# Kernel tuning notes

Measured on AMD Instinct MI355X. Metric: run time of the kernel, lower is better.

## Reference

```python
import jax, jax.numpy as jnp
import numpy as np

B, L, HIDDEN = 64, 200, 256
HEADS = 8
MAX_WIDTH = 5
EPS = 1e-5  # F.layer_norm default eps


def _ln(x):
    # F.layer_norm with no learned affine
    m = jnp.mean(x, axis=-1, keepdims=True)
    v = jnp.mean((x - m) ** 2, axis=-1, keepdims=True)
    return (x - m) * jax.lax.rsqrt(v + EPS)


def _area_pool(x, max_width, mode):
    # x: [B, H, L, D] -> pooled spans of widths 1..max_width (valid windows),
    # concatenated along the memory axis: M = sum_w (L - w + 1)
    Lx = x.shape[2]
    outs = []
    for w in range(1, max_width + 1):
        # [w, B, H, L-w+1, D] stack of shifted slices (w <= 5, tiny loop)
        win = jnp.stack([x[:, :, i:Lx - w + 1 + i, :] for i in range(w)], axis=0)
        if mode == 'max':
            outs.append(win.max(axis=0))
        elif mode == 'mean':
            outs.append(win.mean(axis=0))
        else:  # 'sum'
            outs.append(win.sum(axis=0))
    return jnp.concatenate(outs, axis=2)


def _mha_area(q_in, k_in, v_in, Wq, bq, Wk, bk, Wv, bv, Wo, bo):
    # per-head size equals hidden_size (key_query_size_hidden = hidden_size)
    Bq, Lq, _ = q_in.shape
    Dh = Wq.shape[1] // HEADS

    def split(x):
        return x.reshape(x.shape[0], x.shape[1], HEADS, Dh).transpose(0, 2, 1, 3)

    q = split(q_in @ Wq + bq)  # [B, H, Lq, Dh]
    k = split(k_in @ Wk + bk)
    v = split(v_in @ Wv + bv)
    k_area = _area_pool(k, MAX_WIDTH, 'max')   # aggr='max' key pooling
    v_area = _area_pool(v, MAX_WIDTH, 'sum')   # values pooled by sum (t2t default)
    scale = jnp.asarray(1.0 / np.sqrt(Dh), q.dtype)
    logits = jnp.einsum('bhqd,bhmd->bhqm', q, k_area) * scale
    attn = jax.nn.softmax(logits, axis=-1)  # dropout inactive at eval
    out = jnp.einsum('bhqm,bhmd->bhqd', attn, v_area)
    out = out.transpose(0, 2, 1, 3).reshape(Bq, Lq, HEADS * Dh)
    return out @ Wo + bo


def setup_inputs() -> dict:
    key = jax.random.key(0)
    ks = jax.random.split(key, 16)
    stdv = 1.0 / np.sqrt(HIDDEN)
    u = lambda k, shp: jax.random.uniform(k, shp, jnp.float32, -stdv, stdv)
    HD = HEADS * HIDDEN  # 2048
    return {
        'A': jax.random.normal(ks[0], (B, L, L), jnp.float32),
        'hidden': jax.random.normal(ks[1], (B, L, HIDDEN), jnp.float32),
        'Wq': u(ks[2], (HIDDEN, HD)), 'bq': u(ks[3], (HD,)),
        'Wk': u(ks[4], (HIDDEN, HD)), 'bk': u(ks[5], (HD,)),
        'Wv': u(ks[6], (HIDDEN, HD)), 'bv': u(ks[7], (HD,)),
        'Wo': u(ks[8], (HD, HIDDEN)), 'bo': u(ks[9], (HIDDEN,)),
        'W1': u(ks[10], (HIDDEN, 4 * HIDDEN)), 'b1': u(ks[11], (4 * HIDDEN,)),
        'W2': u(ks[12], (4 * HIDDEN, HIDDEN)), 'b2': u(ks[13], (HIDDEN,)),
    }


def reference(A, hidden, Wq, bq, Wk, bk, Wv, bv, Wo, bo, W1, b1, W2, b2):
    # step = 1 -> single ATTNCell; A is unused by ATTNCell (matches source)
    attn1 = _mha_area(hidden, hidden, hidden, Wq, bq, Wk, bk, Wv, bv, Wo, bo)
    attn1 = _ln(attn1 + hidden)
    attn2 = _mha_area(attn1, hidden, hidden, Wq, bq, Wk, bk, Wv, bv, Wo, bo)
    attn2 = _ln(attn1 + attn2)  # F.dropout inactive (eval)
    x = jax.nn.relu(attn2 @ W1 + b1) @ W2 + b2
    return _ln(attn2 + x)
```

## Files before the change

### kernel.cpp

```cpp
#include <hip/hip_runtime.h>
#include <hip/hip_bf16.h>
#include <cstdint>
#include <cstddef>

#define BATCH 64
#define LSEQ 200
#define HID 256
#define NH 8
#define DH 256
#define HD (NH*DH)
#define MROWS (BATCH*LSEQ)
#define EPS 1e-5f
#define CSCALE 0.09014195f

typedef unsigned short ushort_t;
typedef __attribute__((ext_vector_type(8))) short bf16x8;
typedef __attribute__((ext_vector_type(8))) unsigned short u16x8;
typedef __attribute__((ext_vector_type(4))) float f32x4;

__device__ __forceinline__ float b2f(ushort_t u) {
    union { unsigned int i; float f; } c; c.i = ((unsigned int)u) << 16; return c.f;
}
__device__ __forceinline__ ushort_t f2b(float f) {
    __hip_bfloat16 h = __float2bfloat16(f);
    union { __hip_bfloat16 h; ushort_t u; } c; c.h = h; return c.u;
}
__device__ __forceinline__ float to_f32(float x) { return x; }
__device__ __forceinline__ float to_f32(ushort_t x) { return b2f(x); }
__device__ __forceinline__ void store_val(float* p, float v) { *p = v; }
__device__ __forceinline__ void store_val(ushort_t* p, float v) { *p = f2b(v); }

__device__ __forceinline__ u16x8 bmax8(u16x8 a, u16x8 b) {
    union U { u16x8 v; __hip_bfloat162 h[4]; };
    U ua, ub, r; ua.v = a; ub.v = b;
    #pragma unroll
    for (int i = 0; i < 4; ++i) r.h[i] = __hmax2(ua.h[i], ub.h[i]);
    return r.v;
}

__device__ __forceinline__ void gll16(const void* g, void* l) {
    __builtin_amdgcn_global_load_lds(
        (const __attribute__((address_space(1))) unsigned int*)g,
        (__attribute__((address_space(3))) unsigned int*)l, 16, 0, 0);
}

template<bool RELU, bool SCALEC>
__global__ __launch_bounds__(256) void gemm_bt(
    const ushort_t* __restrict__ A, const ushort_t* __restrict__ Bt,
    const float* __restrict__ bias, ushort_t* __restrict__ C,
    int M, int N, int K)
{
    __shared__ ushort_t As[128 * 64];
    __shared__ ushort_t Bs[128 * 64];
    const int t = threadIdx.x;
    const int m0 = blockIdx.y * 128, n0 = blockIdx.x * 128;
    const int wave = t >> 6, lane = t & 63;
    const int l15 = lane & 15, lq = lane >> 4;
    const int wr = wave >> 1, wc = wave & 1;

    f32x4 acc[4][4];
    #pragma unroll
    for (int i = 0; i < 4; ++i)
        #pragma unroll
        for (int j = 0; j < 4; ++j) acc[i][j] = (f32x4){0.f, 0.f, 0.f, 0.f};

    for (int k0 = 0; k0 < K; k0 += 64) {
        __syncthreads();
        #pragma unroll
        for (int i = 0; i < 4; ++i) {
            int li = i * 256 + t;
            int ml = li >> 3, cp = li & 7;
            int cg = cp ^ (ml & 7);
            gll16(A + (size_t)(m0 + ml) * K + k0 + cg * 8, &As[li * 8]);
        }
        #pragma unroll
        for (int i = 0; i < 4; ++i) {
            int li = i * 256 + t;
            int nl = li >> 3, cp = li & 7;
            int cg = cp ^ (nl & 7);
            gll16(Bt + (size_t)(n0 + nl) * K + k0 + cg * 8, &Bs[li * 8]);
        }
        __syncthreads();
        #pragma unroll
        for (int ks = 0; ks < 2; ++ks) {
            bf16x8 af[4], bfr[4];
            #pragma unroll
            for (int i = 0; i < 4; ++i) {
                int r = wr * 64 + i * 16 + l15;
                int pc = (ks * 4 + lq) ^ (r & 7);
                af[i] = *(const bf16x8*)&As[r * 64 + pc * 8];
            }
            #pragma unroll
            for (int j = 0; j < 4; ++j) {
                int r = wc * 64 + j * 16 + l15;
                int pc = (ks * 4 + lq) ^ (r & 7);
                bfr[j] = *(const bf16x8*)&Bs[r * 64 + pc * 8];
            }
            #pragma unroll
            for (int i = 0; i < 4; ++i)
                #pragma unroll
                for (int j = 0; j < 4; ++j)
                    acc[i][j] = __builtin_amdgcn_mfma_f32_16x16x32_bf16(af[i], bfr[j], acc[i][j], 0, 0, 0);
        }
    }
    #pragma unroll
    for (int i = 0; i < 4; ++i) {
        #pragma unroll
        for (int e = 0; e < 4; ++e) {
            int m = m0 + wr * 64 + i * 16 + 4 * lq + e;
            #pragma unroll
            for (int j = 0; j < 4; ++j) {
                int n = n0 + wc * 64 + j * 16 + l15;
                float v = acc[i][j][e] + bias[n];
                if (RELU) v = fmaxf(v, 0.f);
                if (SCALEC) v *= CSCALE;
                C[(size_t)m * N + n] = f2b(v);
            }
        }
    }
}

__global__ __launch_bounds__(256) void gemm_qkv(
    const ushort_t* __restrict__ A, const ushort_t* __restrict__ Bt,
    const float* __restrict__ bq, const float* __restrict__ bk,
    const float* __restrict__ bv,
    ushort_t* __restrict__ Cq, ushort_t* __restrict__ Ck, ushort_t* __restrict__ Cv)
{
    constexpr int K = HID;
    __shared__ ushort_t As[128 * 64];
    __shared__ ushort_t Bs[128 * 64];
    const int t = threadIdx.x;
    const int m0 = blockIdx.y * 128, n0 = blockIdx.x * 128;
    const int wave = t >> 6, lane = t & 63;
    const int l15 = lane & 15, lq = lane >> 4;
    const int wr = wave >> 1, wc = wave & 1;

    f32x4 acc[4][4];
    #pragma unroll
    for (int i = 0; i < 4; ++i)
        #pragma unroll
        for (int j = 0; j < 4; ++j) acc[i][j] = (f32x4){0.f, 0.f, 0.f, 0.f};

    for (int k0 = 0; k0 < K; k0 += 64) {
        __syncthreads();
        #pragma unroll
        for (int i = 0; i < 4; ++i) {
            int li = i * 256 + t;
            int ml = li >> 3, cp = li & 7;
            int cg = cp ^ (ml & 7);
            gll16(A + (size_t)(m0 + ml) * K + k0 + cg * 8, &As[li * 8]);
        }
        #pragma unroll
        for (int i = 0; i < 4; ++i) {
            int li = i * 256 + t;
            int nl = li >> 3, cp = li & 7;
            int cg = cp ^ (nl & 7);
            gll16(Bt + (size_t)(n0 + nl) * K + k0 + cg * 8, &Bs[li * 8]);
        }
        __syncthreads();
        #pragma unroll
        for (int ks = 0; ks < 2; ++ks) {
            bf16x8 af[4], bfr[4];
            #pragma unroll
            for (int i = 0; i < 4; ++i) {
                int r = wr * 64 + i * 16 + l15;
                int pc = (ks * 4 + lq) ^ (r & 7);
                af[i] = *(const bf16x8*)&As[r * 64 + pc * 8];
            }
            #pragma unroll
            for (int j = 0; j < 4; ++j) {
                int r = wc * 64 + j * 16 + l15;
                int pc = (ks * 4 + lq) ^ (r & 7);
                bfr[j] = *(const bf16x8*)&Bs[r * 64 + pc * 8];
            }
            #pragma unroll
            for (int i = 0; i < 4; ++i)
                #pragma unroll
                for (int j = 0; j < 4; ++j)
                    acc[i][j] = __builtin_amdgcn_mfma_f32_16x16x32_bf16(af[i], bfr[j], acc[i][j], 0, 0, 0);
        }
    }

    const int seg = n0 >> 11;
    const int nb = n0 & 2047;
    if (seg == 2) {
        #pragma unroll
        for (int i = 0; i < 4; ++i) {
            int mbase = m0 + wr * 64 + i * 16 + 4 * lq;
            int bb = (int)(((unsigned)mbase * 5243u) >> 20);
            int ll = mbase - bb * 200;
            #pragma unroll
            for (int j = 0; j < 4; ++j) {
                int nn = nb + wc * 64 + j * 16 + l15;
                float bsv = bv[nn];
                ushort4 o4;
                o4.x = f2b(acc[i][j][0] + bsv); o4.y = f2b(acc[i][j][1] + bsv);
                o4.z = f2b(acc[i][j][2] + bsv); o4.w = f2b(acc[i][j][3] + bsv);
                size_t addr = ((size_t)(bb * NH + (nn >> 8)) * 256 + (nn & 255)) * LSEQ + ll;
                *(ushort4*)&Cv[addr] = o4;
            }
        }
    } else if (seg == 1) {
        #pragma unroll
        for (int i = 0; i < 4; ++i) {
            #pragma unroll
            for (int e = 0; e < 4; ++e) {
                int m = m0 + wr * 64 + i * 16 + 4 * lq + e;
                int bb = (int)(((unsigned)m * 5243u) >> 20);
                int ll = m - bb * 200;
                #pragma unroll
                for (int j = 0; j < 4; ++j) {
                    int nn = nb + wc * 64 + j * 16 + l15;
                    float v = acc[i][j][e] + bk[nn];
                    size_t addr = ((((size_t)(bb * NH + (nn >> 8))) * LSEQ + ll) << 8) + (nn & 255);
                    Ck[addr] = f2b(v);
                }
            }
        }
    } else {
        #pragma unroll
        for (int i = 0; i < 4; ++i) {
            #pragma unroll
            for (int e = 0; e < 4; ++e) {
                int m = m0 + wr * 64 + i * 16 + 4 * lq + e;
                #pragma unroll
                for (int j = 0; j < 4; ++j) {
                    int nn = nb + wc * 64 + j * 16 + l15;
                    float v = (acc[i][j][e] + bq[nn]) * CSCALE;
                    Cq[(size_t)m * HD + nn] = f2b(v);
                }
            }
        }
    }
}

__global__ __launch_bounds__(256) void gemm_bt64(
    const ushort_t* __restrict__ A, const ushort_t* __restrict__ Bt,
    const float* __restrict__ bias, ushort_t* __restrict__ C,
    int M, int N, int K)
{
    __shared__ ushort_t As[64 * 64];
    __shared__ ushort_t Bs[128 * 64];
    const int t = threadIdx.x;
    const int m0 = blockIdx.y * 64, n0 = blockIdx.x * 128;
    const int wave = t >> 6, lane = t & 63;
    const int l15 = lane & 15, lq = lane >> 4;
    const int wr = wave >> 1, wc = wave & 1;

    f32x4 acc[2][4];
    #pragma unroll
    for (int i = 0; i < 2; ++i)
        #pragma unroll
        for (int j = 0; j < 4; ++j) acc[i][j] = (f32x4){0.f, 0.f, 0.f, 0.f};

    for (int k0 = 0; k0 < K; k0 += 64) {
        __syncthreads();
        #pragma unroll
        for (int i = 0; i < 2; ++i) {
            int li = i * 256 + t;
            int ml = li >> 3, cp = li & 7;
            int cg = cp ^ (ml & 7);
            gll16(A + (size_t)(m0 + ml) * K + k0 + cg * 8, &As[li * 8]);
        }
        #pragma unroll
        for (int i = 0; i < 4; ++i) {
            int li = i * 256 + t;
            int nl = li >> 3, cp = li & 7;
            int cg = cp ^ (nl & 7);
            gll16(Bt + (size_t)(n0 + nl) * K + k0 + cg * 8, &Bs[li * 8]);
        }
        __syncthreads();
        #pragma unroll
        for (int ks = 0; ks < 2; ++ks) {
            bf16x8 af[2], bfr[4];
            #pragma unroll
            for (int i = 0; i < 2; ++i) {
                int r = wr * 32 + i * 16 + l15;
                int pc = (ks * 4 + lq) ^ (r & 7);
                af[i] = *(const bf16x8*)&As[r * 64 + pc * 8];
            }
            #pragma unroll
            for (int j = 0; j < 4; ++j) {
                int r = wc * 64 + j * 16 + l15;
                int pc = (ks * 4 + lq) ^ (r & 7);
                bfr[j] = *(const bf16x8*)&Bs[r * 64 + pc * 8];
            }
            #pragma unroll
            for (int i = 0; i < 2; ++i)
                #pragma unroll
                for (int j = 0; j < 4; ++j)
                    acc[i][j] = __builtin_amdgcn_mfma_f32_16x16x32_bf16(af[i], bfr[j], acc[i][j], 0, 0, 0);
        }
    }
    #pragma unroll
    for (int i = 0; i < 2; ++i) {
        #pragma unroll
        for (int e = 0; e < 4; ++e) {
            int m = m0 + wr * 32 + i * 16 + 4 * lq + e;
            #pragma unroll
            for (int j = 0; j < 4; ++j) {
                int n = n0 + wc * 64 + j * 16 + l15;
                C[(size_t)m * N + n] = f2b(acc[i][j][e] + bias[n]);
            }
        }
    }
}

__global__ __launch_bounds__(512, 2) void attn_mfma21(
    const ushort_t* __restrict__ Q, const ushort_t* __restrict__ Khm,
    const ushort_t* __restrict__ Vt, ushort_t* __restrict__ O)
{
    const int id = blockIdx.x;
    const int xcd = id & 7, slot_ = id >> 3;
    const int qt = slot_ & 1;
    const int bh = ((slot_ >> 1) << 3) + xcd;
    const int b = bh >> 3, h = bh & 7;
    const int q0 = qt * 128;
    const int t = threadIdx.x;
    const int wave = t >> 6, lane = t & 63;
    const int l15 = lane & 15, lq = lane >> 4;

    __shared__ ushort_t Ks[64 * 256];
    __shared__ ushort_t Vs[256 * 64];

    const ushort_t* kbh = Khm + (size_t)bh * LSEQ * DH;
    const ushort_t* vtb = Vt + (size_t)bh * DH * LSEQ;
    const ushort_t* qbh = Q + ((size_t)b * LSEQ) * HD + h * DH;
    const int qrow = q0 + wave * 16 + l15;

    bf16x8 qf[8];
    if (qrow < LSEQ) {
        const ushort_t* qp = qbh + (size_t)qrow * HD + 8 * lq;
        #pragma unroll
        for (int g = 0; g < 8; ++g) qf[g] = *(const bf16x8*)(qp + 32 * g);
    } else {
        bf16x8 zf = {0,0,0,0,0,0,0,0};
        #pragma unroll
        for (int g = 0; g < 8; ++g) qf[g] = zf;
    }

    f32x4 oacc[16];
    #pragma unroll
    for (int i = 0; i < 16; ++i) oacc[i] = (f32x4){0.f, 0.f, 0.f, 0.f};
    float l4[4];
    #pragma unroll
    for (int e = 0; e < 4; ++e) l4[e] = 0.f;
    float carry[4];
    #pragma unroll
    for (int e = 0; e < 4; ++e) carry[e] = 0.f;
    float Pagg[4][4];

    const int dc = t & 31, mb = t >> 5;
    const int vd = t >> 1, vh = t & 1;
    const int srow = ((mb >> 2) << 4) + (mb & 3);

    auto kOff = [&](int k4) {
        int m = mb + 16 * k4;
        return m * 256 + ((dc ^ (m & 15)) * 8);
    };
    auto storeVchunk = [&](int kc, u16x8 val) {
        *(u16x8*)&Vs[vd * 64 + ((kc ^ (vd & 7)) * 8)] = val;
    };

    auto qk = [&](f32x4* sacc) {
        __builtin_amdgcn_s_setprio(1);
        #pragma unroll
        for (int ms = 0; ms < 4; ++ms) {
            f32x4 s = (f32x4){0.f, 0.f, 0.f, 0.f};
            const int row = ms * 16 + l15;
            #pragma unroll
            for (int g = 0; g < 8; ++g) {
                const int phys = (lq + 4 * g) ^ l15;
                s = __builtin_amdgcn_mfma_f32_16x16x32_bf16(
                        *(const bf16x8*)&Ks[row * 256 + phys * 8], qf[g], s, 0, 0, 0);
            }
            sacc[ms] = s;
        }
        __builtin_amdgcn_s_setprio(0);
    };

    auto smClass = [&](const f32x4* sacc, int cls) {
        float Pc[4][4];
        #pragma unroll
        for (int ms = 0; ms < 4; ++ms)
            #pragma unroll
            for (int e = 0; e < 4; ++e) {
                float pe = __builtin_exp2f(sacc[ms][e]);
                l4[e] += pe;
                Pc[ms][e] = pe;
                Pagg[ms][e] += pe;
            }
        if (cls >= 1) {
            float T[4][4];
            #pragma unroll
            for (int ms = 0; ms < 4; ++ms)
                #pragma unroll
                for (int e = 0; e < 4; ++e) T[ms][e] = Pc[ms][e];
            #pragma unroll
            for (int u = 1; u <= 4; ++u) {
                if (u <= cls) {
                    float up = __shfl(T[3][3], (lane - 16) & 63);
                    #pragma unroll
                    for (int ms = 3; ms >= 0; --ms) {
                        float nv = (ms > 0) ? T[ms - 1][3] : ((lq > 0) ? up : 0.f);
                        T[ms][3] = T[ms][2]; T[ms][2] = T[ms][1]; T[ms][1] = T[ms][0];
                        T[ms][0] = nv;
                    }
                    #pragma unroll
                    for (int ms = 0; ms < 4; ++ms)
                        #pragma unroll
                        for (int e = 0; e < 4; ++e) Pagg[ms][e] += T[ms][e];
                }
            }
        }
        #pragma unroll
        for (int i = 0; i < 4; ++i)
            #pragma unroll
            for (int e = 0; e < 4; ++e)
                if (cls >= 4 + i - e) carry[i] += Pc[3][e];
    };

    auto pv32 = [&](const float P[4][4]) {
        unsigned int w[8];
        #pragma unroll
        for (int ms = 0; ms < 4; ++ms) {
            asm("v_cvt_pk_bf16_f32 %0, %1, %2" : "=v"(w[2*ms])   : "v"(P[ms][0]), "v"(P[ms][1]));
            asm("v_cvt_pk_bf16_f32 %0, %1, %2" : "=v"(w[2*ms+1]) : "v"(P[ms][2]), "v"(P[ms][3]));
        }
        union FR { unsigned int u[4]; bf16x8 v; };
        FR f0, f1;
        f0.u[0] = w[0]; f0.u[1] = w[1]; f0.u[2] = w[2]; f0.u[3] = w[3];
        f1.u[0] = w[4]; f1.u[1] = w[5]; f1.u[2] = w[6]; f1.u[3] = w[7];
        const bf16x8 pf0 = f0.v, pf1 = f1.v;
        __builtin_amdgcn_s_setprio(1);
        #pragma unroll
        for (int dt = 0; dt < 16; ++dt) {
            const int d = dt * 16 + l15;
            const int p0 = lq ^ (d & 7);
            const int p1 = (lq + 4) ^ (d & 7);
            oacc[dt] = __builtin_amdgcn_mfma_f32_16x16x32_bf16(
                           pf0, *(const bf16x8*)&Vs[d * 64 + p0 * 8], oacc[dt], 0, 0, 0);
            oacc[dt] = __builtin_amdgcn_mfma_f32_16x16x32_bf16(
                           pf1, *(const bf16x8*)&Vs[d * 64 + p1 * 8], oacc[dt], 0, 0, 0);
        }
        __builtin_amdgcn_s_setprio(0);
    };

    for (int ti = 0; ti < 3; ++ti) {
        const int st0 = ti * 64;
        {
            float pin0 = __shfl(carry[0], (lane + 48) & 63);
            float pin1 = __shfl(carry[1], (lane + 48) & 63);
            float pin2 = __shfl(carry[2], (lane + 48) & 63);
            float pin3 = __shfl(carry[3], (lane + 48) & 63);
            #pragma unroll
            for (int ms = 0; ms < 4; ++ms)
                #pragma unroll
                for (int e = 0; e < 4; ++e) Pagg[ms][e] = 0.f;
            if (lq == 0) {
                Pagg[0][0] = pin0; Pagg[0][1] = pin1; Pagg[0][2] = pin2; Pagg[0][3] = pin3;
            }
            #pragma unroll
            for (int e = 0; e < 4; ++e) carry[e] = 0.f;
        }
        #pragma unroll
        for (int cls = 0; cls < 5; ++cls) {
            u16x8 kf[4];
            #pragma unroll
            for (int k4 = 0; k4 < 4; ++k4)
                kf[k4] = *(const u16x8*)(kbh + (size_t)(st0 + srow + 4 * k4 + cls) * DH + dc * 8);
            u16x8 vc[4];
            if (cls == 0) {
                const ushort_t* vrow = vtb + (size_t)vd * LSEQ + st0 + vh * 32;
                #pragma unroll
                for (int c2 = 0; c2 < 4; ++c2) vc[c2] = *(const u16x8*)(vrow + c2 * 8);
            }
            __syncthreads();

            #pragma unroll
            for (int k4 = 0; k4 < 4; ++k4) {
                ushort_t* kp = &Ks[kOff(k4)];
                *(u16x8*)kp = (cls == 0) ? kf[k4] : bmax8(*(const u16x8*)kp, kf[k4]);
            }
            if (cls == 0) {
                #pragma unroll
                for (int cl = 0; cl < 4; ++cl) {
                    const int cg = vh * 4 + cl;
                    storeVchunk((cg & 1) * 4 + (cg >> 1), vc[cl]);
                }
            }
            __syncthreads();

            f32x4 sacc[4];
            qk(sacc);
            smClass(sacc, cls);
            if (cls == 4) pv32(Pagg);
        }
    }

    {
        __syncthreads();
        if (mb < 8) {
            u16x8 krun = *(const u16x8*)(kbh + (size_t)(192 + mb) * DH + dc * 8);
            const u16x8 kz = {0,0,0,0,0,0,0,0};
            #pragma unroll
            for (int k8 = 0; k8 < 8; ++k8) {
                const bool vv = (k8 <= 4) && (mb <= 7 - k8);
                if (k8 > 0 && vv)
                    krun = bmax8(krun, *(const u16x8*)(kbh + (size_t)(192 + mb + k8) * DH + dc * 8));
                int slot = k8 * 8 + mb;
                *(u16x8*)&Ks[slot * 256 + ((dc ^ (slot & 15)) * 8)] = vv ? krun : kz;
            }
        }
        {
            u16x8 v0 = *(const u16x8*)(vtb + (size_t)vd * LSEQ + 192);
            float f[8];
            #pragma unroll
            for (int e = 0; e < 8; ++e) f[e] = b2f(v0[e]);
            #pragma unroll
            for (int ck = 0; ck < 4; ++ck) {
                const int kc = vh * 4 + ck;
                const int cls_lo = 4 * (kc >> 2) + ((kc >> 1) & 1);
                const int offb = 4 * (kc & 1);
                u16x8 ov;
                #pragma unroll
                for (int o = 0; o < 8; ++o) {
                    const int cls = cls_lo + 2 * (o >> 2);
                    const int off = offb + (o & 3);
                    ushort_t val = 0;
                    if (cls <= 4 && off <= 7 - cls) {
                        float a = 0.f;
                        #pragma unroll
                        for (int u = 0; u <= 4; ++u)
                            if (u <= cls) a += f[off + u];
                        val = f2b(a);
                    }
                    if (kc == 6 && o < 4) val = v0[o];
                    ov[o] = val;
                }
                storeVchunk(kc, ov);
            }
        }
        __syncthreads();

        f32x4 sacc[4];
        qk(sacc);
        float pullc[4];
        #pragma unroll
        for (int e = 0; e < 4; ++e) pullc[e] = __shfl(carry[e], (lane + 16) & 63);
        float Pt[4][4];
        #pragma unroll
        for (int ms = 0; ms < 4; ++ms)
            #pragma unroll
            for (int e = 0; e < 4; ++e) {
                const int slot = ms * 16 + 4 * lq + e;
                const bool inval = ((slot & 7) > 7 - (slot >> 3)) || ((slot >> 3) > 4);
                float pe = __builtin_exp2f(inval ? -1e30f : sacc[ms][e]);
                l4[e] += pe;
                float pfrag = pe;
                if (ms == 2 && lq == 2) pfrag = pullc[e];
                Pt[ms][e] = pfrag;
            }
        pv32(Pt);
    }

    float l_part = (l4[0] + l4[1]) + (l4[2] + l4[3]);
    l_part += __shfl_xor(l_part, 16);
    l_part += __shfl_xor(l_part, 32);
    const float inv = 1.f / l_part;

    ushort_t* ob = O + ((size_t)b * LSEQ) * HD + h * DH;
    #pragma unroll
    for (int e = 0; e < 4; ++e) {
        const int q = q0 + wave * 16 + 4 * lq + e;
        const float linv = __shfl(inv, 4 * lq + e);
        if (q < LSEQ) {
            #pragma unroll
            for (int dt = 0; dt < 16; ++dt)
                ob[(size_t)q * HD + dt * 16 + l15] = f2b(oacc[dt][e] * linv);
        }
    }
}

template<typename TR, typename TO>
__global__ __launch_bounds__(256) void residual_ln(
    const ushort_t* __restrict__ X, const TR* __restrict__ R, TO* __restrict__ Out)
{
    const int row = blockIdx.x;
    const int t = threadIdx.x;
    const size_t base = (size_t)row * HID;
    float v = b2f(X[base + t]) + to_f32(R[base + t]);
    float s = v, q = v * v;
    #pragma unroll
    for (int o = 32; o > 0; o >>= 1) {
        s += __shfl_xor(s, o, 64);
        q += __shfl_xor(q, o, 64);
    }
    __shared__ float ss[4], sq[4];
    const int wave = t >> 6, lane = t & 63;
    if (lane == 0) { ss[wave] = s; sq[wave] = q; }
    __syncthreads();
    s = ss[0] + ss[1] + ss[2] + ss[3];
    q = sq[0] + sq[1] + sq[2] + sq[3];
    float mean = s * (1.f / HID);
    float var  = q * (1.f / HID) - mean * mean;
    store_val(&Out[base + t], (v - mean) * rsqrtf(var + EPS));
}

__global__ __launch_bounds__(256) void prep_all(
    const float* __restrict__ hidden, ushort_t* __restrict__ hb,
    const float* __restrict__ Wq, ushort_t* __restrict__ WtQ,
    const float* __restrict__ Wk, ushort_t* __restrict__ WtK,
    const float* __restrict__ Wv, ushort_t* __restrict__ WtV,
    const float* __restrict__ Wo, ushort_t* __restrict__ WtO,
    const float* __restrict__ W1, ushort_t* __restrict__ Wt1,
    const float* __restrict__ W2, ushort_t* __restrict__ Wt2)
{
    __shared__ float tile[32][33];
    int bid = blockIdx.x;
    const int t = threadIdx.x;
    if (bid < 3200) {
        const int i = (bid * 256 + t) * 4;
        float4 v = *(const float4*)(hidden + i);
        ushort4 o;
        o.x = f2b(v.x); o.y = f2b(v.y); o.z = f2b(v.z); o.w = f2b(v.w);
        *(ushort4*)(hb + i) = o;
        return;
    }
    bid -= 3200;
    const float* W; ushort_t* Wt; int K, N;
    if (bid < 512)       {             W = Wq; Wt = WtQ; K = HID;     N = HD;      }
    else if (bid < 1024) { bid -= 512; W = Wk; Wt = WtK; K = HID;     N = HD;      }
    else if (bid < 1536) { bid -= 1024; W = Wv; Wt = WtV; K = HID;    N = HD;      }
    else if (bid < 2048) { bid -= 1536; W = Wo; Wt = WtO; K = HD;     N = HID;     }
    else if (bid < 2304) { bid -= 2048; W = W1; Wt = Wt1; K = HID;    N = 4 * HID; }
    else                 { bid -= 2304; W = W2; Wt = Wt2; K = 4 * HID; N = HID;    }
    const int ntx = N / 32;
    const int n0 = (bid % ntx) * 32, k0 = (bid / ntx) * 32;
    const int tx = t & 31, ty = t >> 5;
    #pragma unroll
    for (int s = 0; s < 4; ++s)
        tile[ty + 8 * s][tx] = W[(size_t)(k0 + ty + 8 * s) * N + n0 + tx];
    __syncthreads();
    #pragma unroll
    for (int s = 0; s < 4; ++s)
        Wt[(size_t)(n0 + ty + 8 * s) * K + k0 + tx] = f2b(tile[tx][ty + 8 * s]);
}

extern "C" void kernel_launch(void* const* d_in, const int* in_sizes, int n_in,
                              void* d_out, int out_size, void* d_ws, size_t ws_size,
                              hipStream_t stream) {
    const float* hidden = (const float*)d_in[1];
    const float* Wq = (const float*)d_in[2];  const float* bq = (const float*)d_in[3];
    const float* Wk = (const float*)d_in[4];  const float* bk = (const float*)d_in[5];
    const float* Wv = (const float*)d_in[6];  const float* bv = (const float*)d_in[7];
    const float* Wo = (const float*)d_in[8];  const float* bo = (const float*)d_in[9];
    const float* W1 = (const float*)d_in[10]; const float* b1 = (const float*)d_in[11];
    const float* W2 = (const float*)d_in[12]; const float* b2 = (const float*)d_in[13];
    float* out = (float*)d_out;

    constexpr size_t SZ_BF   = (size_t)MROWS * HD * 2;
    constexpr size_t SZ_HBF  = (size_t)MROWS * HID * 2;
    constexpr size_t SZ_WQKV = (size_t)HID * HD * 2;
    constexpr size_t SZ_W12  = (size_t)HID * 4 * HID * 2;
    char* ws = (char*)d_ws;
    size_t off = 0;
    ushort_t* kb   = (ushort_t*)(ws + off); off += SZ_BF;
    ushort_t* vt   = (ushort_t*)(ws + off); off += SZ_BF;
    ushort_t* qo   = (ushort_t*)(ws + off); off += SZ_BF;
    ushort_t* hb   = (ushort_t*)(ws + off); off += SZ_HBF;
    ushort_t* at1  = (ushort_t*)(ws + off); off += SZ_HBF;
    ushort_t* at2  = (ushort_t*)(ws + off); off += SZ_HBF;
    ushort_t* proj = (ushort_t*)(ws + off); off += SZ_HBF;
    ushort_t* WtQ  = (ushort_t*)(ws + off); off += SZ_WQKV;
    ushort_t* WtK  = (ushort_t*)(ws + off); off += SZ_WQKV;
    ushort_t* WtV  = (ushort_t*)(ws + off); off += SZ_WQKV;
    ushort_t* WtO  = (ushort_t*)(ws + off); off += SZ_WQKV;
    ushort_t* Wt1  = (ushort_t*)(ws + off); off += SZ_W12;
    ushort_t* Wt2  = (ushort_t*)(ws + off); off += SZ_W12;
    if (ws_size < off) return;
    ushort_t* ffn1 = qo;

    dim3 blk(256);
    prep_all<<<5760, blk, 0, stream>>>(hidden, hb, Wq, WtQ, Wk, WtK, Wv, WtV,
                                       Wo, WtO, W1, Wt1, W2, Wt2);

    const dim3 gQKV(3 * HD / 128, MROWS / 128);
    const dim3 gProj(HD / 128, MROWS / 128);
    const dim3 gOut64(HID / 128, MROWS / 64);
    const dim3 gF1(4 * HID / 128, MROWS / 128);

    gemm_qkv<<<gQKV, blk, 0, stream>>>(hb, WtQ, bq, bk, bv, qo, kb, vt);

    attn_mfma21<<<2 * BATCH * NH, 512, 0, stream>>>(qo, kb, vt, qo);
    gemm_bt64<<<gOut64, blk, 0, stream>>>(qo, WtO, bo, proj, MROWS, HID, HD);
    residual_ln<float, ushort_t><<<MROWS, blk, 0, stream>>>(proj, hidden, at1);

    gemm_bt<false, true><<<gProj, blk, 0, stream>>>(at1, WtQ, bq, qo, MROWS, HD, HID);
    attn_mfma21<<<2 * BATCH * NH, 512, 0, stream>>>(qo, kb, vt, qo);
    gemm_bt64<<<gOut64, blk, 0, stream>>>(qo, WtO, bo, proj, MROWS, HID, HD);
    residual_ln<ushort_t, ushort_t><<<MROWS, blk, 0, stream>>>(proj, at1, at2);

    gemm_bt<true, false><<<gF1, blk, 0, stream>>>(at2, Wt1, b1, ffn1, MROWS, 4 * HID, HID);
    gemm_bt64<<<gOut64, blk, 0, stream>>>(ffn1, Wt2, b2, proj, MROWS, HID, 4 * HID);
    residual_ln<ushort_t, float><<<MROWS, blk, 0, stream>>>(proj, at2, out);
}
```

Measured before the change: 833.9 us.

## Fuse output-projection GEMMs with residual add and LayerNorm epilogue

Replaces the 64x128-tiled output GEMM plus the separate residual_ln kernel with one kernel. Each 512-thread block computes a full 64x256 row tile, so it can add bias and residual and do the LayerNorm reduction in its epilogue through shuffles and a small shared-memory exchange. This removes the bf16 round trip through the proj buffer and three kernel launches, and keeps LN precision in fp32. In exchange there are half as many blocks (200 instead of 400), which means lower parallelism on a large GPU, and each block carries a larger B tile in LDS.

```diff
diff --git a/kernel.cpp b/kernel.cpp
--- a/kernel.cpp
+++ b/kernel.cpp
@@ -234,18 +234,20 @@
     }
 }
 
-__global__ __launch_bounds__(256) void gemm_bt64(
+template<typename TR, typename TO>
+__global__ __launch_bounds__(512, 2) void gemm_out_ln(
     const ushort_t* __restrict__ A, const ushort_t* __restrict__ Bt,
-    const float* __restrict__ bias, ushort_t* __restrict__ C,
-    int M, int N, int K)
+    const float* __restrict__ bias, const TR* __restrict__ R,
+    TO* __restrict__ Out, int K)
 {
     __shared__ ushort_t As[64 * 64];
-    __shared__ ushort_t Bs[128 * 64];
+    __shared__ ushort_t Bs[256 * 64];
+    __shared__ float rs[64][4], rq[64][4];
     const int t = threadIdx.x;
-    const int m0 = blockIdx.y * 64, n0 = blockIdx.x * 128;
+    const int m0 = blockIdx.x * 64;
     const int wave = t >> 6, lane = t & 63;
     const int l15 = lane & 15, lq = lane >> 4;
-    const int wr = wave >> 1, wc = wave & 1;
+    const int wr = wave >> 2, wc = wave & 3;
 
     f32x4 acc[2][4];
     #pragma unroll
@@ -255,19 +257,17 @@
 
     for (int k0 = 0; k0 < K; k0 += 64) {
         __syncthreads();
-        #pragma unroll
-        for (int i = 0; i < 2; ++i) {
-            int li = i * 256 + t;
-            int ml = li >> 3, cp = li & 7;
+        {
+            int ml = t >> 3, cp = t & 7;
             int cg = cp ^ (ml & 7);
-            gll16(A + (size_t)(m0 + ml) * K + k0 + cg * 8, &As[li * 8]);
+            gll16(A + (size_t)(m0 + ml) * K + k0 + cg * 8, &As[t * 8]);
         }
         #pragma unroll
         for (int i = 0; i < 4; ++i) {
-            int li = i * 256 + t;
+            int li = i * 512 + t;
             int nl = li >> 3, cp = li & 7;
             int cg = cp ^ (nl & 7);
-            gll16(Bt + (size_t)(n0 + nl) * K + k0 + cg * 8, &Bs[li * 8]);
+            gll16(Bt + (size_t)nl * K + k0 + cg * 8, &Bs[li * 8]);
         }
         __syncthreads();
         #pragma unroll
@@ -292,18 +292,54 @@
                     acc[i][j] = __builtin_amdgcn_mfma_f32_16x16x32_bf16(af[i], bfr[j], acc[i][j], 0, 0, 0);
         }
     }
-    #pragma unroll
-    for (int i = 0; i < 2; ++i) {
+
+    float v[2][4][4];
+    #pragma unroll
+    for (int i = 0; i < 2; ++i)
         #pragma unroll
         for (int e = 0; e < 4; ++e) {
-            int m = m0 + wr * 32 + i * 16 + 4 * lq + e;
+            const int m = m0 + wr * 32 + i * 16 + 4 * lq + e;
             #pragma unroll
             for (int j = 0; j < 4; ++j) {
-                int n = n0 + wc * 64 + j * 16 + l15;
-                C[(size_t)m * N + n] = f2b(acc[i][j][e] + bias[n]);
-            }
-        }
-    }
+                const int n = wc * 64 + j * 16 + l15;
+                v[i][j][e] = acc[i][j][e] + bias[n] + to_f32(R[(size_t)m * HID + n]);
+            }
+        }
+    #pragma unroll
+    for (int i = 0; i < 2; ++i)
+        #pragma unroll
+        for (int e = 0; e < 4; ++e) {
+            float s = (v[i][0][e] + v[i][1][e]) + (v[i][2][e] + v[i][3][e]);
+            float q = (v[i][0][e] * v[i][0][e] + v[i][1][e] * v[i][1][e])
+                    + (v[i][2][e] * v[i][2][e] + v[i][3][e] * v[i][3][e]);
+            #pragma unroll
+            for (int o = 1; o < 16; o <<= 1) {
+                s += __shfl_xor(s, o);
+                q += __shfl_xor(q, o);
+            }
+            if (l15 == 0) {
+                const int row = wr * 32 + i * 16 + 4 * lq + e;
+                rs[row][wc] = s; rq[row][wc] = q;
+            }
+        }
+    __syncthreads();
+    #pragma unroll
+    for (int i = 0; i < 2; ++i)
+        #pragma unroll
+        for (int e = 0; e < 4; ++e) {
+            const int row = wr * 32 + i * 16 + 4 * lq + e;
+            const float s = (rs[row][0] + rs[row][1]) + (rs[row][2] + rs[row][3]);
+            const float q = (rq[row][0] + rq[row][1]) + (rq[row][2] + rq[row][3]);
+            const float mean = s * (1.f / HID);
+            const float var  = q * (1.f / HID) - mean * mean;
+            const float rstd = rsqrtf(var + EPS);
+            const int m = m0 + row;
+            #pragma unroll
+            for (int j = 0; j < 4; ++j) {
+                const int n = wc * 64 + j * 16 + l15;
+                store_val(&Out[(size_t)m * HID + n], (v[i][j][e] - mean) * rstd);
+            }
+        }
 }
 
 __global__ __launch_bounds__(512, 2) void attn_mfma21(
@@ -580,31 +616,6 @@
                 ob[(size_t)q * HD + dt * 16 + l15] = f2b(oacc[dt][e] * linv);
         }
     }
-}
-
-template<typename TR, typename TO>
-__global__ __launch_bounds__(256) void residual_ln(
-    const ushort_t* __restrict__ X, const TR* __restrict__ R, TO* __restrict__ Out)
-{
-    const int row = blockIdx.x;
-    const int t = threadIdx.x;
-    const size_t base = (size_t)row * HID;
-    float v = b2f(X[base + t]) + to_f32(R[base + t]);
-    float s = v, q = v * v;
-    #pragma unroll
-    for (int o = 32; o > 0; o >>= 1) {
-        s += __shfl_xor(s, o, 64);
-        q += __shfl_xor(q, o, 64);
-    }
-    __shared__ float ss[4], sq[4];
-    const int wave = t >> 6, lane = t & 63;
-    if (lane == 0) { ss[wave] = s; sq[wave] = q; }
-    __syncthreads();
-    s = ss[0] + ss[1] + ss[2] + ss[3];
-    q = sq[0] + sq[1] + sq[2] + sq[3];
-    float mean = s * (1.f / HID);
-    float var  = q * (1.f / HID) - mean * mean;
-    store_val(&Out[base + t], (v - mean) * rsqrtf(var + EPS));
 }
 
 __global__ __launch_bounds__(256) void prep_all(
@@ -680,6 +691,7 @@
     ushort_t* Wt2  = (ushort_t*)(ws + off); off += SZ_W12;
     if (ws_size < off) return;
     ushort_t* ffn1 = qo;
+    (void)proj;
 
     dim3 blk(256);
     prep_all<<<5760, blk, 0, stream>>>(hidden, hb, Wq, WtQ, Wk, WtK, Wv, WtV,
@@ -687,21 +699,17 @@
 
     const dim3 gQKV(3 * HD / 128, MROWS / 128);
     const dim3 gProj(HD / 128, MROWS / 128);
-    const dim3 gOut64(HID / 128, MROWS / 64);
     const dim3 gF1(4 * HID / 128, MROWS / 128);
 
     gemm_qkv<<<gQKV, blk, 0, stream>>>(hb, WtQ, bq, bk, bv, qo, kb, vt);
 
     attn_mfma21<<<2 * BATCH * NH, 512, 0, stream>>>(qo, kb, vt, qo);
-    gemm_bt64<<<gOut64, blk, 0, stream>>>(qo, WtO, bo, proj, MROWS, HID, HD);
-    residual_ln<float, ushort_t><<<MROWS, blk, 0, stream>>>(proj, hidden, at1);
+    gemm_out_ln<float, ushort_t><<<MROWS / 64, 512, 0, stream>>>(qo, WtO, bo, hidden, at1, HD);
 
     gemm_bt<false, true><<<gProj, blk, 0, stream>>>(at1, WtQ, bq, qo, MROWS, HD, HID);
     attn_mfma21<<<2 * BATCH * NH, 512, 0, stream>>>(qo, kb, vt, qo);
-    gemm_bt64<<<gOut64, blk, 0, stream>>>(qo, WtO, bo, proj, MROWS, HID, HD);
-    residual_ln<ushort_t, ushort_t><<<MROWS, blk, 0, stream>>>(proj, at1, at2);
+    gemm_out_ln<ushort_t, ushort_t><<<MROWS / 64, 512, 0, stream>>>(qo, WtO, bo, at1, at2, HD);
 
     gemm_bt<true, false><<<gF1, blk, 0, stream>>>(at2, Wt1, b1, ffn1, MROWS, 4 * HID, HID);
-    gemm_bt64<<<gOut64, blk, 0, stream>>>(ffn1, Wt2, b2, proj, MROWS, HID, 4 * HID);
-    residual_ln<ushort_t, float><<<MROWS, blk, 0, stream>>>(proj, at2, out);
-}
+    gemm_out_ln<ushort_t, float><<<MROWS / 64, 512, 0, stream>>>(ffn1, Wt2, b2, at2, out, 4 * HID);
+}
```

New measurement: 814.5 us. 2.3% less time.
